# Kernel tuning notes

Measured on AMD Instinct MI355X. Metric: run time of the kernel, lower is better.

Reference implementation:

```python
import jax, jax.numpy as jnp
import numpy as np

N = 50000      # nodes
E = 800000     # edges
D_IN, D_HID, D_MID, D_OUT = 128, 128, 30, 64  # layer dims (30 hard-coded in module)
NEG_SLOPE = 0.01  # F.leaky_relu default

def _w(key, shape, scale=0.05):
    return jax.random.normal(key, shape, dtype=jnp.float32) * scale

def setup_inputs() -> dict:
    key = jax.random.key(0)
    ks = jax.random.split(key, 24)
    inp = {
        "x": jax.random.normal(ks[0], (N, D_IN), jnp.float32),
        "e": jax.random.normal(ks[1], (E, D_IN), jnp.float32),
        "src": jax.random.randint(ks[2], (E,), 0, N, jnp.int32),
        "dst": jax.random.randint(ks[3], (E,), 0, N, jnp.int32),
    }
    dims = [(D_IN, D_HID), (D_HID, D_MID), (D_MID, D_OUT)]
    i = 4
    for l, (di, do) in enumerate(dims, 1):
        inp[f"W_n{l}"] = _w(ks[i], (di, do)); i += 1
        inp[f"b_n{l}"] = jnp.zeros((do,), jnp.float32)
        inp[f"W_ni{l}"] = _w(ks[i], (di, do)); i += 1
        inp[f"W_nj{l}"] = _w(ks[i], (di, do)); i += 1
        inp[f"W_f{l}"] = _w(ks[i], (di, do)); i += 1
        inp[f"attn{l}"] = _w(ks[i], (do,)); i += 1
        inp[f"bias{l}"] = jnp.zeros((do,), jnp.float32)
    return inp

def _egat_layer(x, e, src, dst, W_n, b_n, W_ni, W_nj, W_f, attn, bias):
    n = x.shape[0]
    # edge features: f_ij = leaky_relu(fc_ni(x)_i + fc_nj(x)_j + fc_fij(e) + bias)
    f = (x @ W_ni)[src] + (x @ W_nj)[dst] + e @ W_f + bias
    f = jax.nn.leaky_relu(f, negative_slope=NEG_SLOPE)          # [E, do]
    score = jnp.sum(f * attn, axis=-1)                           # [E]
    # edge_softmax: softmax of scores over edges sharing a destination node
    m = jax.ops.segment_max(score, dst, num_segments=n)
    ex = jnp.exp(score - m[dst])
    s = jax.ops.segment_sum(ex, dst, num_segments=n)
    a = ex / s[dst]                                              # [E]
    # attention-weighted aggregation of transformed source nodes
    h = x @ W_n + b_n                                            # [N, do]
    h_out = jax.ops.segment_sum(h[src] * a[:, None], dst, num_segments=n)
    return h_out, f

def reference(x, e, src, dst,
              W_n1, b_n1, W_ni1, W_nj1, W_f1, attn1, bias1,
              W_n2, b_n2, W_ni2, W_nj2, W_f2, attn2, bias2,
              W_n3, b_n3, W_ni3, W_nj3, W_f3, attn3, bias3):
    h, f = _egat_layer(x, e, src, dst, W_n1, b_n1, W_ni1, W_nj1, W_f1, attn1, bias1)
    h, f = _egat_layer(h, f, src, dst, W_n2, b_n2, W_ni2, W_nj2, W_f2, attn2, bias2)
    h, f = _egat_layer(h, f, src, dst, W_n3, b_n3, W_ni3, W_nj3, W_f3, attn3, bias3)
    # num_heads == 1, so out_edge_feats[:, 0, :] == f  -> [E, D_OUT]
    return f
```

## Files before the change

### kernel.cpp

```cpp
#include <hip/hip_runtime.h>
#include <math.h>

#define NTH 256

__device__ __forceinline__ unsigned enc_f(float x){
  unsigned u = __float_as_uint(x);
  return (u & 0x80000000u) ? ~u : (u | 0x80000000u);
}
__device__ __forceinline__ float dec_f(unsigned v){
  unsigned u = (v & 0x80000000u) ? (v & 0x7FFFFFFFu) : ~v;
  return __uint_as_float(u);
}

template<int DI, int DIS, int DO, int DOS, int MINW>
__global__ __launch_bounds__(NTH, MINW) void node_linear_k(
    const float* __restrict__ x, const float* __restrict__ W,
    const float* __restrict__ bias, float* __restrict__ out, int N)
{
  const int lane = threadIdx.x & 63;
  const int wave = threadIdx.x >> 6;
  const int row = (blockIdx.x * (NTH >> 6) + wave) * 64 + lane;
  const bool valid = row < N;
  const int rr = valid ? row : (N - 1);
  const float* xr = x + (size_t)rr * DIS;

  float acc[DO];
  if (bias != nullptr) {
    #pragma unroll
    for (int j = 0; j < DO; j++) acc[j] = bias[j];
  } else {
    #pragma unroll
    for (int j = 0; j < DO; j++) acc[j] = 0.f;
  }

  constexpr int K4 = DI & ~3;
  for (int k = 0; k < K4; k += 4) {
    float4 ev = *(const float4*)(xr + k);
    float ea[4] = {ev.x, ev.y, ev.z, ev.w};
    #pragma unroll
    for (int kk = 0; kk < 4; kk++) {
      const float* wr = W + (size_t)(k + kk) * DO;
      #pragma unroll
      for (int j = 0; j < DO; j++)
        acc[j] = fmaf(ea[kk], wr[j], acc[j]);
    }
  }
  #pragma unroll
  for (int k = K4; k < DI; k++) {
    float ev = xr[k];
    const float* wr = W + (size_t)k * DO;
    #pragma unroll
    for (int j = 0; j < DO; j++)
      acc[j] = fmaf(ev, wr[j], acc[j]);
  }

  if (valid) {
    float* orow = out + (size_t)row * DOS;
    constexpr int J4 = DO & ~3;
    #pragma unroll
    for (int j = 0; j < J4; j += 4)
      *(float4*)(orow + j) = make_float4(acc[j], acc[j+1], acc[j+2], acc[j+3]);
    #pragma unroll
    for (int j = J4; j < DO; j++) orow[j] = acc[j];
  }
}

template<int DI, int DIS, int DO, int DOS, bool SCORE, int MINW>
__global__ __launch_bounds__(NTH, MINW) void edge_f_k(
    const float* __restrict__ efeat, const float* __restrict__ xWni,
    const float* __restrict__ xWnj, const float* __restrict__ Wf,
    const float* __restrict__ attn, const float* __restrict__ bias,
    const int* __restrict__ src, const int* __restrict__ dst,
    float* __restrict__ fout, float* __restrict__ score,
    unsigned* __restrict__ menc, int E)
{
  const int lane = threadIdx.x & 63;
  const int wave = threadIdx.x >> 6;
  const int eidx = (blockIdx.x * (NTH >> 6) + wave) * 64 + lane;
  const bool valid = eidx < E;
  const int ee = valid ? eidx : (E - 1);

  const int sn = src[ee];
  const int dn = dst[ee];
  const float* ar = xWni + (size_t)sn * DOS;
  const float* br = xWnj + (size_t)dn * DOS;

  float acc[DO];
  constexpr int J4 = DO & ~3;
  #pragma unroll
  for (int j = 0; j < J4; j += 4) {
    float4 a4 = *(const float4*)(ar + j);
    float4 b4 = *(const float4*)(br + j);
    acc[j+0] = bias[j+0] + a4.x + b4.x;
    acc[j+1] = bias[j+1] + a4.y + b4.y;
    acc[j+2] = bias[j+2] + a4.z + b4.z;
    acc[j+3] = bias[j+3] + a4.w + b4.w;
  }
  #pragma unroll
  for (int j = J4; j < DO; j++)
    acc[j] = bias[j] + ar[j] + br[j];

  const float* er = efeat + (size_t)ee * DIS;
  constexpr int K4 = DI & ~3;
  for (int k = 0; k < K4; k += 4) {
    float4 ev = *(const float4*)(er + k);
    float ea[4] = {ev.x, ev.y, ev.z, ev.w};
    #pragma unroll
    for (int kk = 0; kk < 4; kk++) {
      const float* wr = Wf + (size_t)(k + kk) * DO;
      #pragma unroll
      for (int j = 0; j < DO; j++)
        acc[j] = fmaf(ea[kk], wr[j], acc[j]);
    }
  }
  #pragma unroll
  for (int k = K4; k < DI; k++) {
    float ev = er[k];
    const float* wr = Wf + (size_t)k * DO;
    #pragma unroll
    for (int j = 0; j < DO; j++)
      acc[j] = fmaf(ev, wr[j], acc[j]);
  }

  float sc = 0.f;
  #pragma unroll
  for (int j = 0; j < DO; j++) {
    float v = acc[j];
    v = (v > 0.f) ? v : 0.01f * v;
    acc[j] = v;
    if (SCORE) sc += v * attn[j];
  }

  if (valid) {
    float* orow = fout + (size_t)eidx * DOS;
    #pragma unroll
    for (int j = 0; j < J4; j += 4)
      *(float4*)(orow + j) = make_float4(acc[j], acc[j+1], acc[j+2], acc[j+3]);
    #pragma unroll
    for (int j = J4; j < DO; j++) orow[j] = acc[j];
    if constexpr (SCORE) {
      score[eidx] = sc;
      atomicMax(&menc[dn], enc_f(sc));
    }
  }
}

__global__ __launch_bounds__(NTH) void softmax_ex_k(float* __restrict__ score,
    const int* __restrict__ dst, const unsigned* __restrict__ menc,
    float* __restrict__ ssum, int E)
{
  int i = blockIdx.x * NTH + threadIdx.x;
  if (i < E) {
    int d = dst[i];
    float ex = expf(score[i] - dec_f(menc[d]));
    score[i] = ex;
    atomicAdd(&ssum[d], ex);
  }
}

__global__ __launch_bounds__(NTH) void softmax_norm_k(float* __restrict__ score,
    const float* __restrict__ ssum, const int* __restrict__ dst, int E)
{
  int i = blockIdx.x * NTH + threadIdx.x;
  if (i < E) score[i] = score[i] / ssum[dst[i]];
}

template<int DO, int HS, int OS>
__global__ __launch_bounds__(NTH) void scatter_h_k(const float* __restrict__ a,
    const int* __restrict__ src, const int* __restrict__ dst,
    const float* __restrict__ h, float* __restrict__ hout, int E)
{
  long long idx = (long long)blockIdx.x * NTH + threadIdx.x;
  if (idx < (long long)E * DO) {
    int e = (int)(idx / DO);
    int col = (int)(idx - (long long)e * DO);
    atomicAdd(&hout[(size_t)dst[e] * OS + col], h[(size_t)src[e] * HS + col] * a[e]);
  }
}

extern "C" void kernel_launch(void* const* d_in, const int* in_sizes, int n_in,
                              void* d_out, int out_size, void* d_ws, size_t ws_size,
                              hipStream_t stream)
{
  const float* x    = (const float*)d_in[0];
  const float* e    = (const float*)d_in[1];
  const int*   src  = (const int*)d_in[2];
  const int*   dst  = (const int*)d_in[3];
  const float* W_n1 = (const float*)d_in[4];   const float* b_n1  = (const float*)d_in[5];
  const float* W_ni1= (const float*)d_in[6];   const float* W_nj1 = (const float*)d_in[7];
  const float* W_f1 = (const float*)d_in[8];   const float* attn1 = (const float*)d_in[9];
  const float* bias1= (const float*)d_in[10];
  const float* W_n2 = (const float*)d_in[11];  const float* b_n2  = (const float*)d_in[12];
  const float* W_ni2= (const float*)d_in[13];  const float* W_nj2 = (const float*)d_in[14];
  const float* W_f2 = (const float*)d_in[15];  const float* attn2 = (const float*)d_in[16];
  const float* bias2= (const float*)d_in[17];
  const float* W_n3 = (const float*)d_in[18];  const float* b_n3  = (const float*)d_in[19];
  const float* W_ni3= (const float*)d_in[20];  const float* W_nj3 = (const float*)d_in[21];
  const float* W_f3 = (const float*)d_in[22];  const float* attn3 = (const float*)d_in[23];
  const float* bias3= (const float*)d_in[24];
  (void)W_n3; (void)b_n3;

  const int N = in_sizes[0] / 128;
  const int E = in_sizes[2];

  float* ws = (float*)d_ws;
  size_t off = 0;
  float* fbuf1 = ws + off; off += (size_t)E * 128;
  float* fbuf2 = ws + off; off += (size_t)E * 32;
  float* xWni  = ws + off; off += (size_t)N * 128;
  float* xWnj  = ws + off; off += (size_t)N * 128;
  float* hbuf  = ws + off; off += (size_t)N * 128;
  float* nodeA = ws + off; off += (size_t)N * 128;
  float* nodeB = ws + off; off += (size_t)N * 32;
  float* scoreb= ws + off; off += (size_t)E;
  unsigned* menc = (unsigned*)(ws + off); off += (size_t)N;
  float* sbuf  = ws + off; off += (size_t)N;

  const int gN = (N + NTH - 1) / NTH;
  const int gEe = (E + NTH - 1) / NTH;
  const int gE = gEe;

  node_linear_k<128,128,128,128,2><<<gN,NTH,0,stream>>>(x, W_ni1, nullptr, xWni, N);
  node_linear_k<128,128,128,128,2><<<gN,NTH,0,stream>>>(x, W_nj1, nullptr, xWnj, N);
  node_linear_k<128,128,128,128,2><<<gN,NTH,0,stream>>>(x, W_n1,  b_n1,   hbuf, N);
  hipMemsetAsync(menc, 0, (size_t)N * 4, stream);
  hipMemsetAsync(sbuf, 0, (size_t)N * 4, stream);
  hipMemsetAsync(nodeA, 0, (size_t)N * 128 * 4, stream);
  edge_f_k<128,128,128,128,true,2><<<gE,NTH,0,stream>>>(e, xWni, xWnj, W_f1, attn1, bias1,
                                                        src, dst, fbuf1, scoreb, menc, E);
  softmax_ex_k<<<gEe,NTH,0,stream>>>(scoreb, dst, menc, sbuf, E);
  softmax_norm_k<<<gEe,NTH,0,stream>>>(scoreb, sbuf, dst, E);
  scatter_h_k<128,128,128><<<(int)(((long long)E*128 + NTH-1)/NTH),NTH,0,stream>>>(scoreb, src, dst, hbuf, nodeA, E);

  node_linear_k<128,128,30,32,4><<<gN,NTH,0,stream>>>(nodeA, W_ni2, nullptr, xWni, N);
  node_linear_k<128,128,30,32,4><<<gN,NTH,0,stream>>>(nodeA, W_nj2, nullptr, xWnj, N);
  node_linear_k<128,128,30,32,4><<<gN,NTH,0,stream>>>(nodeA, W_n2,  b_n2,   hbuf, N);
  hipMemsetAsync(menc, 0, (size_t)N * 4, stream);
  hipMemsetAsync(sbuf, 0, (size_t)N * 4, stream);
  hipMemsetAsync(nodeB, 0, (size_t)N * 32 * 4, stream);
  edge_f_k<128,128,30,32,true,4><<<gE,NTH,0,stream>>>(fbuf1, xWni, xWnj, W_f2, attn2, bias2,
                                                      src, dst, fbuf2, scoreb, menc, E);
  softmax_ex_k<<<gEe,NTH,0,stream>>>(scoreb, dst, menc, sbuf, E);
  softmax_norm_k<<<gEe,NTH,0,stream>>>(scoreb, sbuf, dst, E);
  scatter_h_k<30,32,32><<<(int)(((long long)E*30 + NTH-1)/NTH),NTH,0,stream>>>(scoreb, src, dst, hbuf, nodeB, E);

  node_linear_k<30,32,64,64,3><<<gN,NTH,0,stream>>>(nodeB, W_ni3, nullptr, xWni, N);
  node_linear_k<30,32,64,64,3><<<gN,NTH,0,stream>>>(nodeB, W_nj3, nullptr, xWnj, N);
  edge_f_k<30,32,64,64,false,3><<<gE,NTH,0,stream>>>(fbuf2, xWni, xWnj, W_f3, attn3, bias3,
                                                     src, dst, (float*)d_out, nullptr, nullptr, E);
}
```

Baseline: 3.031 ms.

## Split output columns across waves to cut per-thread accumulators and raise occupancy

```diff
diff --git a/kernel.cpp b/kernel.cpp
--- a/kernel.cpp
+++ b/kernel.cpp
@@ -12,25 +12,30 @@
   return __uint_as_float(u);
 }
 
-template<int DI, int DIS, int DO, int DOS, int MINW>
+template<int DI, int DIS, int DO, int DOS, int JSPLIT, int MINW>
 __global__ __launch_bounds__(NTH, MINW) void node_linear_k(
     const float* __restrict__ x, const float* __restrict__ W,
     const float* __restrict__ bias, float* __restrict__ out, int N)
 {
+  constexpr int WPB = NTH / 64;
+  constexpr int GPB = WPB / JSPLIT;
+  constexpr int DOW = DO / JSPLIT;
   const int lane = threadIdx.x & 63;
   const int wave = threadIdx.x >> 6;
-  const int row = (blockIdx.x * (NTH >> 6) + wave) * 64 + lane;
+  const int group = blockIdx.x * GPB + (wave / JSPLIT);
+  const int j0 = __builtin_amdgcn_readfirstlane((wave % JSPLIT) * DOW);
+  const int row = group * 64 + lane;
   const bool valid = row < N;
   const int rr = valid ? row : (N - 1);
   const float* xr = x + (size_t)rr * DIS;
 
-  float acc[DO];
+  float acc[DOW];
   if (bias != nullptr) {
     #pragma unroll
-    for (int j = 0; j < DO; j++) acc[j] = bias[j];
+    for (int j = 0; j < DOW; j++) acc[j] = bias[j0 + j];
   } else {
     #pragma unroll
-    for (int j = 0; j < DO; j++) acc[j] = 0.f;
+    for (int j = 0; j < DOW; j++) acc[j] = 0.f;
   }
 
   constexpr int K4 = DI & ~3;
@@ -39,33 +44,33 @@
     float ea[4] = {ev.x, ev.y, ev.z, ev.w};
     #pragma unroll
     for (int kk = 0; kk < 4; kk++) {
-      const float* wr = W + (size_t)(k + kk) * DO;
+      const float* wr = W + (size_t)(k + kk) * DO + j0;
       #pragma unroll
-      for (int j = 0; j < DO; j++)
+      for (int j = 0; j < DOW; j++)
         acc[j] = fmaf(ea[kk], wr[j], acc[j]);
     }
   }
   #pragma unroll
   for (int k = K4; k < DI; k++) {
     float ev = xr[k];
-    const float* wr = W + (size_t)k * DO;
-    #pragma unroll
-    for (int j = 0; j < DO; j++)
+    const float* wr = W + (size_t)k * DO + j0;
+    #pragma unroll
+    for (int j = 0; j < DOW; j++)
       acc[j] = fmaf(ev, wr[j], acc[j]);
   }
 
   if (valid) {
-    float* orow = out + (size_t)row * DOS;
-    constexpr int J4 = DO & ~3;
+    float* orow = out + (size_t)row * DOS + j0;
+    constexpr int J4 = DOW & ~3;
     #pragma unroll
     for (int j = 0; j < J4; j += 4)
       *(float4*)(orow + j) = make_float4(acc[j], acc[j+1], acc[j+2], acc[j+3]);
     #pragma unroll
-    for (int j = J4; j < DO; j++) orow[j] = acc[j];
-  }
-}
-
-template<int DI, int DIS, int DO, int DOS, bool SCORE, int MINW>
+    for (int j = J4; j < DOW; j++) orow[j] = acc[j];
+  }
+}
+
+template<int DI, int DIS, int DO, int DOS, int JSPLIT, bool SCORE, int MINW>
 __global__ __launch_bounds__(NTH, MINW) void edge_f_k(
     const float* __restrict__ efeat, const float* __restrict__ xWni,
     const float* __restrict__ xWnj, const float* __restrict__ Wf,
@@ -74,31 +79,37 @@
     float* __restrict__ fout, float* __restrict__ score,
     unsigned* __restrict__ menc, int E)
 {
+  constexpr int WPB = NTH / 64;
+  constexpr int GPB = WPB / JSPLIT;
+  constexpr int DOW = DO / JSPLIT;
   const int lane = threadIdx.x & 63;
   const int wave = threadIdx.x >> 6;
-  const int eidx = (blockIdx.x * (NTH >> 6) + wave) * 64 + lane;
+  const int sub  = wave % JSPLIT;
+  const int group = blockIdx.x * GPB + (wave / JSPLIT);
+  const int j0 = __builtin_amdgcn_readfirstlane(sub * DOW);
+  const int eidx = group * 64 + lane;
   const bool valid = eidx < E;
   const int ee = valid ? eidx : (E - 1);
 
   const int sn = src[ee];
   const int dn = dst[ee];
-  const float* ar = xWni + (size_t)sn * DOS;
-  const float* br = xWnj + (size_t)dn * DOS;
-
-  float acc[DO];
-  constexpr int J4 = DO & ~3;
+  const float* ar = xWni + (size_t)sn * DOS + j0;
+  const float* br = xWnj + (size_t)dn * DOS + j0;
+
+  float acc[DOW];
+  constexpr int J4 = DOW & ~3;
   #pragma unroll
   for (int j = 0; j < J4; j += 4) {
     float4 a4 = *(const float4*)(ar + j);
     float4 b4 = *(const float4*)(br + j);
-    acc[j+0] = bias[j+0] + a4.x + b4.x;
-    acc[j+1] = bias[j+1] + a4.y + b4.y;
-    acc[j+2] = bias[j+2] + a4.z + b4.z;
-    acc[j+3] = bias[j+3] + a4.w + b4.w;
-  }
-  #pragma unroll
-  for (int j = J4; j < DO; j++)
-    acc[j] = bias[j] + ar[j] + br[j];
+    acc[j+0] = bias[j0+j+0] + a4.x + b4.x;
+    acc[j+1] = bias[j0+j+1] + a4.y + b4.y;
+    acc[j+2] = bias[j0+j+2] + a4.z + b4.z;
+    acc[j+3] = bias[j0+j+3] + a4.w + b4.w;
+  }
+  #pragma unroll
+  for (int j = J4; j < DOW; j++)
+    acc[j] = bias[j0+j] + ar[j] + br[j];
 
   const float* er = efeat + (size_t)ee * DIS;
   constexpr int K4 = DI & ~3;
@@ -107,38 +118,52 @@
     float ea[4] = {ev.x, ev.y, ev.z, ev.w};
     #pragma unroll
     for (int kk = 0; kk < 4; kk++) {
-      const float* wr = Wf + (size_t)(k + kk) * DO;
+      const float* wr = Wf + (size_t)(k + kk) * DO + j0;
       #pragma unroll
-      for (int j = 0; j < DO; j++)
+      for (int j = 0; j < DOW; j++)
         acc[j] = fmaf(ea[kk], wr[j], acc[j]);
     }
   }
   #pragma unroll
   for (int k = K4; k < DI; k++) {
     float ev = er[k];
-    const float* wr = Wf + (size_t)k * DO;
-    #pragma unroll
-    for (int j = 0; j < DO; j++)
+    const float* wr = Wf + (size_t)k * DO + j0;
+    #pragma unroll
+    for (int j = 0; j < DOW; j++)
       acc[j] = fmaf(ev, wr[j], acc[j]);
   }
 
   float sc = 0.f;
   #pragma unroll
-  for (int j = 0; j < DO; j++) {
+  for (int j = 0; j < DOW; j++) {
     float v = acc[j];
     v = (v > 0.f) ? v : 0.01f * v;
     acc[j] = v;
-    if (SCORE) sc += v * attn[j];
+    if (SCORE) sc += v * attn[j0 + j];
   }
 
   if (valid) {
-    float* orow = fout + (size_t)eidx * DOS;
+    float* orow = fout + (size_t)eidx * DOS + j0;
     #pragma unroll
     for (int j = 0; j < J4; j += 4)
       *(float4*)(orow + j) = make_float4(acc[j], acc[j+1], acc[j+2], acc[j+3]);
     #pragma unroll
-    for (int j = J4; j < DO; j++) orow[j] = acc[j];
-    if constexpr (SCORE) {
+    for (int j = J4; j < DOW; j++) orow[j] = acc[j];
+  }
+
+  if constexpr (SCORE && JSPLIT > 1) {
+    __shared__ float scpart[WPB][64];
+    scpart[wave][lane] = sc;
+    __syncthreads();
+    if (sub == 0 && valid) {
+      float tot = sc;
+      #pragma unroll
+      for (int s = 1; s < JSPLIT; s++) tot += scpart[wave + s][lane];
+      score[eidx] = tot;
+      atomicMax(&menc[dn], enc_f(tot));
+    }
+  } else if constexpr (SCORE) {
+    if (valid) {
       score[eidx] = sc;
       atomicMax(&menc[dn], enc_f(sc));
     }
@@ -216,36 +241,40 @@
   unsigned* menc = (unsigned*)(ws + off); off += (size_t)N;
   float* sbuf  = ws + off; off += (size_t)N;
 
-  const int gN = (N + NTH - 1) / NTH;
+  const int groupsN = (N + 63) / 64;
+  const int groupsE = (E + 63) / 64;
+  const int gN2 = (groupsN + 1) / 2;
+  const int gN4 = (groupsN + 3) / 4;
+  const int gE2 = (groupsE + 1) / 2;
+  const int gE4 = (groupsE + 3) / 4;
   const int gEe = (E + NTH - 1) / NTH;
-  const int gE = gEe;
-
-  node_linear_k<128,128,128,128,2><<<gN,NTH,0,stream>>>(x, W_ni1, nullptr, xWni, N);
-  node_linear_k<128,128,128,128,2><<<gN,NTH,0,stream>>>(x, W_nj1, nullptr, xWnj, N);
-  node_linear_k<128,128,128,128,2><<<gN,NTH,0,stream>>>(x, W_n1,  b_n1,   hbuf, N);
+
+  node_linear_k<128,128,128,128,2,4><<<gN2,NTH,0,stream>>>(x, W_ni1, nullptr, xWni, N);
+  node_linear_k<128,128,128,128,2,4><<<gN2,NTH,0,stream>>>(x, W_nj1, nullptr, xWnj, N);
+  node_linear_k<128,128,128,128,2,4><<<gN2,NTH,0,stream>>>(x, W_n1,  b_n1,   hbuf, N);
   hipMemsetAsync(menc, 0, (size_t)N * 4, stream);
   hipMemsetAsync(sbuf, 0, (size_t)N * 4, stream);
   hipMemsetAsync(nodeA, 0, (size_t)N * 128 * 4, stream);
-  edge_f_k<128,128,128,128,true,2><<<gE,NTH,0,stream>>>(e, xWni, xWnj, W_f1, attn1, bias1,
-                                                        src, dst, fbuf1, scoreb, menc, E);
+  edge_f_k<128,128,128,128,2,true,4><<<gE2,NTH,0,stream>>>(e, xWni, xWnj, W_f1, attn1, bias1,
+                                                           src, dst, fbuf1, scoreb, menc, E);
   softmax_ex_k<<<gEe,NTH,0,stream>>>(scoreb, dst, menc, sbuf, E);
   softmax_norm_k<<<gEe,NTH,0,stream>>>(scoreb, sbuf, dst, E);
   scatter_h_k<128,128,128><<<(int)(((long long)E*128 + NTH-1)/NTH),NTH,0,stream>>>(scoreb, src, dst, hbuf, nodeA, E);
 
-  node_linear_k<128,128,30,32,4><<<gN,NTH,0,stream>>>(nodeA, W_ni2, nullptr, xWni, N);
-  node_linear_k<128,128,30,32,4><<<gN,NTH,0,stream>>>(nodeA, W_nj2, nullptr, xWnj, N);
-  node_linear_k<128,128,30,32,4><<<gN,NTH,0,stream>>>(nodeA, W_n2,  b_n2,   hbuf, N);
+  node_linear_k<128,128,30,32,1,5><<<gN4,NTH,0,stream>>>(nodeA, W_ni2, nullptr, xWni, N);
+  node_linear_k<128,128,30,32,1,5><<<gN4,NTH,0,stream>>>(nodeA, W_nj2, nullptr, xWnj, N);
+  node_linear_k<128,128,30,32,1,5><<<gN4,NTH,0,stream>>>(nodeA, W_n2,  b_n2,   hbuf, N);
   hipMemsetAsync(menc, 0, (size_t)N * 4, stream);
   hipMemsetAsync(sbuf, 0, (size_t)N * 4, stream);
   hipMemsetAsync(nodeB, 0, (size_t)N * 32 * 4, stream);
-  edge_f_k<128,128,30,32,true,4><<<gE,NTH,0,stream>>>(fbuf1, xWni, xWnj, W_f2, attn2, bias2,
-                                                      src, dst, fbuf2, scoreb, menc, E);
+  edge_f_k<128,128,30,32,1,true,5><<<gE4,NTH,0,stream>>>(fbuf1, xWni, xWnj, W_f2, attn2, bias2,
+                                                         src, dst, fbuf2, scoreb, menc, E);
   softmax_ex_k<<<gEe,NTH,0,stream>>>(scoreb, dst, menc, sbuf, E);
   softmax_norm_k<<<gEe,NTH,0,stream>>>(scoreb, sbuf, dst, E);
   scatter_h_k<30,32,32><<<(int)(((long long)E*30 + NTH-1)/NTH),NTH,0,stream>>>(scoreb, src, dst, hbuf, nodeB, E);
 
-  node_linear_k<30,32,64,64,3><<<gN,NTH,0,stream>>>(nodeB, W_ni3, nullptr, xWni, N);
-  node_linear_k<30,32,64,64,3><<<gN,NTH,0,stream>>>(nodeB, W_nj3, nullptr, xWnj, N);
-  edge_f_k<30,32,64,64,false,3><<<gE,NTH,0,stream>>>(fbuf2, xWni, xWnj, W_f3, attn3, bias3,
-                                                     src, dst, (float*)d_out, nullptr, nullptr, E);
-}
+  node_linear_k<30,32,64,64,2,4><<<gN2,NTH,0,stream>>>(nodeB, W_ni3, nullptr, xWni, N);
+  node_linear_k<30,32,64,64,2,4><<<gN2,NTH,0,stream>>>(nodeB, W_nj3, nullptr, xWnj, N);
+  edge_f_k<30,32,64,64,2,false,4><<<gE2,NTH,0,stream>>>(fbuf2, xWni, xWnj, W_f3, attn3, bias3,
+                                                        src, dst, (float*)d_out, nullptr, nullptr, E);
+}
```

Measured after the change: 2.634 ms. 13.1% less time.
